# Optimization experiments

Measured on AMD Instinct MI355X. Metric: run time of the kernel, lower is better.

Reference implementation:

```python
import jax, jax.numpy as jnp
import numpy as np

N_NODES = 100000
N_EDGES = 3200000


def _gcn_conv(x, src, dst, W, b, n_nodes):
    # PyG GCNConv: out = D^{-1/2} (A + I) D^{-1/2} X W + b
    h = x @ W  # [N, out]
    # degree of (A + I) counted at targets (symmetric graph assumption as in PyG norm)
    deg = jax.ops.segment_sum(jnp.ones_like(dst, dtype=h.dtype), dst, num_segments=n_nodes)
    dinv = jnp.where(deg > 0, jax.lax.rsqrt(deg), 0.0)
    norm = dinv[src] * dinv[dst]  # [E_total]
    msg = h[src] * norm[:, None]  # gather + normalize  [E_total, out]
    out = jax.ops.segment_sum(msg, dst, num_segments=n_nodes)  # scatter-add
    return out + b


def setup_inputs() -> dict:
    key = jax.random.key(0)
    k1, k2, k3, k4 = jax.random.split(key, 4)
    x = jax.random.normal(k1, (N_NODES, 1), dtype=jnp.float32)
    edge_index = jax.random.randint(k2, (2, N_EDGES), 0, N_NODES, dtype=jnp.int64)
    W1 = jax.random.normal(k3, (1, 64), dtype=jnp.float32) * (1.0 / np.sqrt(1.0))
    b1 = jnp.zeros((64,), dtype=jnp.float32)
    W2 = jax.random.normal(k4, (64, 2), dtype=jnp.float32) * (1.0 / np.sqrt(64.0))
    b2 = jnp.zeros((2,), dtype=jnp.float32)
    return {"x": x, "edge_index": edge_index, "W1": W1, "b1": b1, "W2": W2, "b2": b2}


def reference(x, edge_index, W1, b1, W2, b2):
    n = x.shape[0]
    # add self-loops as GCNConv does by default
    loops = jnp.arange(n, dtype=edge_index.dtype)
    src = jnp.concatenate([edge_index[0], loops])
    dst = jnp.concatenate([edge_index[1], loops])
    h = _gcn_conv(x, src, dst, W1, b1, n)
    h = jax.nn.relu(h)
    h = _gcn_conv(h, src, dst, W2, b2, n)
    h = jax.nn.log_softmax(h, axis=1)
    out = jnp.mean(h, axis=0)
    return out[None, :]  # [1, 2]
```

## Files before the change

### kernel.cpp

```cpp
#include <hip/hip_runtime.h>


#define TPB 256
#define SORT_BLK 256
#define BSHIFT 7
#define BNODES 128
#define MAXBUCK 1024
#define BSTRIDE 6144


__global__ __launch_bounds__(TPB) void k_sort(const int* __restrict__ ei, int E, int epb,
                                              int nbuck, int* __restrict__ gcur,
                                              unsigned* __restrict__ packed) {
    __shared__ int h[MAXBUCK];
    for (int b = threadIdx.x; b < nbuck; b += TPB) h[b] = 0;
    __syncthreads();
    const int4* d4 = (const int4*)(ei + E);
    int nq = epb >> 2;
    int q0 = blockIdx.x * nq;
    for (int j = threadIdx.x; j < nq; j += TPB) {
        int q = q0 + j;
        int e = q << 2;
        if (e + 3 < E) {
            int4 v = d4[q];
            atomicAdd(&h[v.x >> BSHIFT], 1);
            atomicAdd(&h[v.y >> BSHIFT], 1);
            atomicAdd(&h[v.z >> BSHIFT], 1);
            atomicAdd(&h[v.w >> BSHIFT], 1);
        } else {
            for (int k = 0; k < 4; ++k)
                if (e + k < E) atomicAdd(&h[(ei + E)[e + k] >> BSHIFT], 1);
        }
    }
    __syncthreads();
    for (int b = threadIdx.x; b < nbuck; b += TPB) {
        int c = h[b];
        h[b] = c ? atomicAdd(&gcur[b], c) : 0;
    }
    __syncthreads();
    const int4* s4 = (const int4*)ei;
    for (int j = threadIdx.x; j < nq; j += TPB) {
        int q = q0 + j;
        int e = q << 2;
        if (e + 3 < E) {
            int4 vs = s4[q];
            int4 vd = d4[q];
            int b, p;
            b = vd.x >> BSHIFT; p = atomicAdd(&h[b], 1);
            packed[b * BSTRIDE + p] = ((unsigned)(vd.x & (BNODES - 1)) << 17) | (unsigned)vs.x;
            b = vd.y >> BSHIFT; p = atomicAdd(&h[b], 1);
            packed[b * BSTRIDE + p] = ((unsigned)(vd.y & (BNODES - 1)) << 17) | (unsigned)vs.y;
            b = vd.z >> BSHIFT; p = atomicAdd(&h[b], 1);
            packed[b * BSTRIDE + p] = ((unsigned)(vd.z & (BNODES - 1)) << 17) | (unsigned)vs.z;
            b = vd.w >> BSHIFT; p = atomicAdd(&h[b], 1);
            packed[b * BSTRIDE + p] = ((unsigned)(vd.w & (BNODES - 1)) << 17) | (unsigned)vs.w;
        } else {
            for (int k = 0; k < 4; ++k) {
                int ee = e + k;
                if (ee < E) {
                    int s = ei[ee], d = ei[E + ee];
                    int b = d >> BSHIFT;
                    int p = atomicAdd(&h[b], 1);
                    packed[b * BSTRIDE + p] = ((unsigned)(d & (BNODES - 1)) << 17) | (unsigned)s;
                }
            }
        }
    }
}


__global__ __launch_bounds__(TPB) void k_deg_u(const unsigned* __restrict__ packed,
                                               const int* __restrict__ gcur,
                                               const float* __restrict__ x,
                                               float* __restrict__ dinv,
                                               float* __restrict__ u, int N) {
    __shared__ int cnt[4][BNODES];
    for (int k = threadIdx.x; k < 4 * BNODES; k += TPB) ((int*)cnt)[k] = 0;
    __syncthreads();
    int b = blockIdx.x;
    int sz = gcur[b];
    const unsigned* base = packed + (size_t)b * BSTRIDE;
    const uint4* base4 = (const uint4*)base;
    int wv = threadIdx.x >> 6;
    int nq = sz >> 2;
    for (int j = threadIdx.x; j < nq; j += TPB) {
        uint4 p = base4[j];
        atomicAdd(&cnt[wv][(p.x >> 17) & 127], 1);
        atomicAdd(&cnt[wv][(p.y >> 17) & 127], 1);
        atomicAdd(&cnt[wv][(p.z >> 17) & 127], 1);
        atomicAdd(&cnt[wv][(p.w >> 17) & 127], 1);
    }
    int tail = sz & 3;
    if (threadIdx.x < tail) {
        unsigned p = base[(nq << 2) + threadIdx.x];
        atomicAdd(&cnt[wv][(p >> 17) & 127], 1);
    }
    __syncthreads();
    if (threadIdx.x < BNODES) {
        int t = threadIdx.x;
        int node = (b << BSHIFT) + t;
        if (node < N) {
            int deg = cnt[0][t] + cnt[1][t] + cnt[2][t] + cnt[3][t];
            float di = rsqrtf((float)(deg + 1));
            dinv[node] = di;
            u[node] = di * x[node];
        }
    }
}

__global__ __launch_bounds__(TPB) void k_agg1(const unsigned* __restrict__ packed,
                                              const int* __restrict__ gcur,
                                              const float* __restrict__ dinv,
                                              const float* __restrict__ u,
                                              const float* __restrict__ W1,
                                              const float* __restrict__ b1,
                                              const float* __restrict__ W2,
                                              float2* __restrict__ w, int N) {
    __shared__ float acc[4][BNODES];
    __shared__ float sW1[64], sb1[64], sW2[128];
    if (threadIdx.x < 64) { sW1[threadIdx.x] = W1[threadIdx.x]; sb1[threadIdx.x] = b1[threadIdx.x]; }
    if (threadIdx.x < 128) sW2[threadIdx.x] = W2[threadIdx.x];
    for (int k = threadIdx.x; k < 4 * BNODES; k += TPB) ((float*)acc)[k] = 0.f;
    __syncthreads();
    int b = blockIdx.x;
    int sz = gcur[b];
    const unsigned* base = packed + (size_t)b * BSTRIDE;
    const uint4* base4 = (const uint4*)base;
    int wv = threadIdx.x >> 6;
    int nq = sz >> 2;
    for (int j = threadIdx.x; j < nq; j += TPB) {
        uint4 p = base4[j];
        float v0 = u[p.x & 0x1FFFF];
        float v1 = u[p.y & 0x1FFFF];
        float v2 = u[p.z & 0x1FFFF];
        float v3 = u[p.w & 0x1FFFF];
        atomicAdd(&acc[wv][(p.x >> 17) & 127], v0);
        atomicAdd(&acc[wv][(p.y >> 17) & 127], v1);
        atomicAdd(&acc[wv][(p.z >> 17) & 127], v2);
        atomicAdd(&acc[wv][(p.w >> 17) & 127], v3);
    }
    int tail = sz & 3;
    if (threadIdx.x < tail) {
        unsigned p = base[(nq << 2) + threadIdx.x];
        atomicAdd(&acc[wv][(p >> 17) & 127], u[p & 0x1FFFF]);
    }
    __syncthreads();
    if (threadIdx.x < BNODES) {
        int t = threadIdx.x;
        int node = (b << BSHIFT) + t;
        if (node < N) {
            float di = dinv[node];
            float sv = di * (acc[0][t] + acc[1][t] + acc[2][t] + acc[3][t] + u[node]);
            float z0 = 0.f, z1 = 0.f;
            #pragma unroll
            for (int j = 0; j < 64; ++j) {
                float h = fmaxf(fmaf(sv, sW1[j], sb1[j]), 0.f);
                z0 = fmaf(h, sW2[2 * j], z0);
                z1 = fmaf(h, sW2[2 * j + 1], z1);
            }
            w[node] = make_float2(di * z0, di * z1);
        }
    }
}

__global__ __launch_bounds__(TPB) void k_agg2(const unsigned* __restrict__ packed,
                                              const int* __restrict__ gcur,
                                              const float* __restrict__ dinv,
                                              const float2* __restrict__ w,
                                              const float* __restrict__ b2,
                                              float* __restrict__ accum, int N) {
    __shared__ float accx[4][BNODES], accy[4][BNODES];
    for (int k = threadIdx.x; k < 4 * BNODES; k += TPB) {
        ((float*)accx)[k] = 0.f;
        ((float*)accy)[k] = 0.f;
    }
    __syncthreads();
    int b = blockIdx.x;
    int sz = gcur[b];
    const unsigned* base = packed + (size_t)b * BSTRIDE;
    const uint4* base4 = (const uint4*)base;
    int wv = threadIdx.x >> 6;
    int nq = sz >> 2;
    for (int j = threadIdx.x; j < nq; j += TPB) {
        uint4 p = base4[j];
        float2 v0 = w[p.x & 0x1FFFF];
        float2 v1 = w[p.y & 0x1FFFF];
        float2 v2 = w[p.z & 0x1FFFF];
        float2 v3 = w[p.w & 0x1FFFF];
        int l0 = (p.x >> 17) & 127, l1 = (p.y >> 17) & 127;
        int l2 = (p.z >> 17) & 127, l3 = (p.w >> 17) & 127;
        atomicAdd(&accx[wv][l0], v0.x); atomicAdd(&accy[wv][l0], v0.y);
        atomicAdd(&accx[wv][l1], v1.x); atomicAdd(&accy[wv][l1], v1.y);
        atomicAdd(&accx[wv][l2], v2.x); atomicAdd(&accy[wv][l2], v2.y);
        atomicAdd(&accx[wv][l3], v3.x); atomicAdd(&accy[wv][l3], v3.y);
    }
    int tail = sz & 3;
    if (threadIdx.x < tail) {
        unsigned p = base[(nq << 2) + threadIdx.x];
        float2 v = w[p & 0x1FFFF];
        int l = (p >> 17) & 127;
        atomicAdd(&accx[wv][l], v.x);
        atomicAdd(&accy[wv][l], v.y);
    }
    __syncthreads();
    float l0 = 0.f, l1 = 0.f;
    if (threadIdx.x < BNODES) {
        int t = threadIdx.x;
        int node = (b << BSHIFT) + t;
        if (node < N) {
            float di = dinv[node];
            float2 wi = w[node];
            float a0 = di * (accx[0][t] + accx[1][t] + accx[2][t] + accx[3][t] + wi.x) + b2[0];
            float a1 = di * (accy[0][t] + accy[1][t] + accy[2][t] + accy[3][t] + wi.y) + b2[1];
            float m = fmaxf(a0, a1);
            float lse = m + logf(expf(a0 - m) + expf(a1 - m));
            l0 = a0 - lse;
            l1 = a1 - lse;
        }
    }
    #pragma unroll
    for (int off = 32; off > 0; off >>= 1) {
        l0 += __shfl_down(l0, off, 64);
        l1 += __shfl_down(l1, off, 64);
    }
    __shared__ float s0[TPB / 64], s1[TPB / 64];
    int wid = threadIdx.x >> 6, lane = threadIdx.x & 63;
    if (lane == 0) { s0[wid] = l0; s1[wid] = l1; }
    __syncthreads();
    if (threadIdx.x == 0) {
        float t0 = 0.f, t1 = 0.f;
        #pragma unroll
        for (int k = 0; k < TPB / 64; ++k) { t0 += s0[k]; t1 += s1[k]; }
        atomicAdd(&accum[0], t0);
        atomicAdd(&accum[1], t1);
    }
}

__global__ void k_finalize(const float* __restrict__ accum, float* __restrict__ out, float invN) {
    out[0] = accum[0] * invN;
    out[1] = accum[1] * invN;
}


__global__ void k_hist(const int* __restrict__ dst, int E, int* __restrict__ deg) {
    int e = blockIdx.x * TPB + threadIdx.x;
    if (e < E) atomicAdd(&deg[dst[e]], 1);
}
__global__ void k_dinv_u(const int* __restrict__ deg, const float* __restrict__ x,
                         float* __restrict__ dinv, float* __restrict__ u, int N) {
    int i = blockIdx.x * TPB + threadIdx.x;
    if (i < N) {
        float di = rsqrtf((float)(deg[i] + 1));
        dinv[i] = di;
        u[i] = di * x[i];
    }
}
__global__ void k_scatter1(const int* __restrict__ ei, int E,
                           const float* __restrict__ u, float* __restrict__ t) {
    int e = blockIdx.x * TPB + threadIdx.x;
    if (e < E) atomicAdd(&t[ei[E + e]], u[ei[e]]);
}
__global__ void k_node_mid_fb(const float* __restrict__ dinv, const float* __restrict__ u,
                              const float* __restrict__ t,
                              const float* __restrict__ W1, const float* __restrict__ b1,
                              const float* __restrict__ W2, float2* __restrict__ w, int N) {
    __shared__ float sW1[64], sb1[64], sW2[128];
    if (threadIdx.x < 64) { sW1[threadIdx.x] = W1[threadIdx.x]; sb1[threadIdx.x] = b1[threadIdx.x]; }
    if (threadIdx.x < 128) sW2[threadIdx.x] = W2[threadIdx.x];
    __syncthreads();
    int i = blockIdx.x * TPB + threadIdx.x;
    if (i < N) {
        float di = dinv[i];
        float s = di * (t[i] + u[i]);
        float z0 = 0.f, z1 = 0.f;
        #pragma unroll
        for (int j = 0; j < 64; ++j) {
            float h = fmaxf(fmaf(s, sW1[j], sb1[j]), 0.f);
            z0 = fmaf(h, sW2[2 * j], z0);
            z1 = fmaf(h, sW2[2 * j + 1], z1);
        }
        w[i] = make_float2(di * z0, di * z1);
    }
}
__global__ void k_scatter2(const int* __restrict__ ei, int E,
                           const float2* __restrict__ w, float* __restrict__ acc) {
    int e = blockIdx.x * TPB + threadIdx.x;
    if (e < E) {
        float2 ws = w[ei[e]];
        int d = ei[E + e];
        atomicAdd(&acc[2 * d], ws.x);
        atomicAdd(&acc[2 * d + 1], ws.y);
    }
}
__global__ void k_node_out_fb(const float* __restrict__ dinv, const float2* __restrict__ w,
                              const float2* __restrict__ acc, const float* __restrict__ b2,
                              float* __restrict__ accum, int N) {
    int i = blockIdx.x * TPB + threadIdx.x;
    float l0 = 0.f, l1 = 0.f;
    if (i < N) {
        float di = dinv[i];
        float2 a = acc[i];
        float2 ww = w[i];
        float a0 = di * (a.x + ww.x) + b2[0];
        float a1 = di * (a.y + ww.y) + b2[1];
        float m = fmaxf(a0, a1);
        float lse = m + logf(expf(a0 - m) + expf(a1 - m));
        l0 = a0 - lse;
        l1 = a1 - lse;
    }
    #pragma unroll
    for (int off = 32; off > 0; off >>= 1) {
        l0 += __shfl_down(l0, off, 64);
        l1 += __shfl_down(l1, off, 64);
    }
    __shared__ float s0[TPB / 64], s1[TPB / 64];
    int wid = threadIdx.x >> 6, lane = threadIdx.x & 63;
    if (lane == 0) { s0[wid] = l0; s1[wid] = l1; }
    __syncthreads();
    if (threadIdx.x == 0) {
        float t0 = 0.f, t1 = 0.f;
        #pragma unroll
        for (int k = 0; k < TPB / 64; ++k) { t0 += s0[k]; t1 += s1[k]; }
        atomicAdd(&accum[0], t0);
        atomicAdd(&accum[1], t1);
    }
}

extern "C" void kernel_launch(void* const* d_in, const int* in_sizes, int n_in,
                              void* d_out, int out_size, void* d_ws, size_t ws_size,
                              hipStream_t stream) {
    const float* x  = (const float*)d_in[0];
    const int*   ei = (const int*)d_in[1];
    const float* W1 = (const float*)d_in[2];
    const float* b1 = (const float*)d_in[3];
    const float* W2 = (const float*)d_in[4];
    const float* b2 = (const float*)d_in[5];
    float* out = (float*)d_out;

    const int N = in_sizes[0];
    const int E = in_sizes[1] / 2;
    const int nbuck = (N + BNODES - 1) >> BSHIFT;
    const int gridN = (N + TPB - 1) / TPB;
    const int gridE = (E + TPB - 1) / TPB;

    size_t offPacked = 0;
    size_t offW      = offPacked + (size_t)nbuck * BSTRIDE * 4;
    size_t offDinv   = offW + (size_t)N * 8;
    size_t offU      = offDinv + (size_t)N * 4;
    size_t offGcur   = offU + (size_t)N * 4;
    size_t offAccum  = offGcur + (size_t)nbuck * 4;
    size_t need      = offAccum + 8;

    if (ws_size >= need && nbuck <= MAXBUCK && N <= (1 << 17)) {
        unsigned* packed = (unsigned*)((char*)d_ws + offPacked);
        float2*   w      = (float2*)((char*)d_ws + offW);
        float*    dinv   = (float*)((char*)d_ws + offDinv);
        float*    u      = (float*)((char*)d_ws + offU);
        int*      gcur   = (int*)((char*)d_ws + offGcur);
        float*    accum  = (float*)((char*)d_ws + offAccum);

        hipMemsetAsync(gcur, 0, (size_t)nbuck * 4 + 8, stream);

        int epb = (((E + SORT_BLK - 1) / SORT_BLK) + 3) & ~3;

        k_sort<<<SORT_BLK, TPB, 0, stream>>>(ei, E, epb, nbuck, gcur, packed);
        k_deg_u<<<nbuck, TPB, 0, stream>>>(packed, gcur, x, dinv, u, N);
        k_agg1<<<nbuck, TPB, 0, stream>>>(packed, gcur, dinv, u, W1, b1, W2, w, N);
        k_agg2<<<nbuck, TPB, 0, stream>>>(packed, gcur, dinv, (const float2*)w, b2, accum, N);
        k_finalize<<<1, 64, 0, stream>>>(accum, out, 1.0f / (float)N);
    } else {
        int*   deg   = (int*)d_ws;
        float* t     = (float*)(deg + N);
        float* acc   = t + N;
        float* accum = acc + 2 * N;
        float* dinv  = accum + 2;
        float* u     = dinv + N;
        float2* w    = (float2*)(u + N);
        hipMemsetAsync(d_ws, 0, (size_t)(4 * N + 2) * sizeof(float), stream);
        k_hist<<<gridE, TPB, 0, stream>>>(ei + E, E, deg);
        k_dinv_u<<<gridN, TPB, 0, stream>>>(deg, x, dinv, u, N);
        k_scatter1<<<gridE, TPB, 0, stream>>>(ei, E, u, t);
        k_node_mid_fb<<<gridN, TPB, 0, stream>>>(dinv, u, t, W1, b1, W2, w, N);
        k_scatter2<<<gridE, TPB, 0, stream>>>(ei, E, w, acc);
        k_node_out_fb<<<gridN, TPB, 0, stream>>>(dinv, w, (const float2*)acc, b2, accum, N);
        k_finalize<<<1, 64, 0, stream>>>(accum, out, 1.0f / (float)N);
    }
}
```

Before: 193.7 us.

## Sub-sort buckets by source chunk and stage gathers through shared memory

The degree kernel now also sorts each destination bucket's edges by source-node chunk of 4096 nodes and records per-bucket chunk offsets. Both aggregation kernels walk the chunks, stage the chunk's u or w values into LDS, and gather from LDS instead of doing random global loads. The aim is to replace scattered global gathers with coalesced staging loads. The cost is that every block stages all 25 chunks (about 100K floats or float2s per block across roughly 780 blocks), which adds a lot of redundant global traffic, plus extra syncs, a serial scan, and the loss of uint4-vectorised edge reads.

```diff
diff --git a/kernel.cpp b/kernel.cpp
--- a/kernel.cpp
+++ b/kernel.cpp
@@ -7,6 +7,9 @@
 #define BNODES 128
 #define MAXBUCK 1024
 #define BSTRIDE 6144
+#define CSHIFT 12
+#define CSZ 4096
+#define MAXCHUNK 32
 
 
 __global__ __launch_bounds__(TPB) void k_sort(const int* __restrict__ ei, int E, int epb,
@@ -69,53 +72,75 @@
 }
 
 
-__global__ __launch_bounds__(TPB) void k_deg_u(const unsigned* __restrict__ packed,
+__global__ __launch_bounds__(TPB) void k_sort2(unsigned* __restrict__ packed,
                                                const int* __restrict__ gcur,
                                                const float* __restrict__ x,
                                                float* __restrict__ dinv,
-                                               float* __restrict__ u, int N) {
-    __shared__ int cnt[4][BNODES];
-    for (int k = threadIdx.x; k < 4 * BNODES; k += TPB) ((int*)cnt)[k] = 0;
+                                               float* __restrict__ u,
+                                               int* __restrict__ chunkOff,
+                                               int nchunk, int N) {
+    __shared__ unsigned wbuf[BSTRIDE];
+    __shared__ int cntc[4][MAXCHUNK];
+    __shared__ int cntd[4][BNODES];
+    __shared__ int scanA[MAXCHUNK + 1];
+    __shared__ int cur[MAXCHUNK];
+    int wv = threadIdx.x >> 6;
+    for (int k = threadIdx.x; k < 4 * MAXCHUNK; k += TPB) ((int*)cntc)[k] = 0;
+    for (int k = threadIdx.x; k < 4 * BNODES; k += TPB) ((int*)cntd)[k] = 0;
     __syncthreads();
     int b = blockIdx.x;
     int sz = gcur[b];
-    const unsigned* base = packed + (size_t)b * BSTRIDE;
-    const uint4* base4 = (const uint4*)base;
-    int wv = threadIdx.x >> 6;
-    int nq = sz >> 2;
-    for (int j = threadIdx.x; j < nq; j += TPB) {
-        uint4 p = base4[j];
-        atomicAdd(&cnt[wv][(p.x >> 17) & 127], 1);
-        atomicAdd(&cnt[wv][(p.y >> 17) & 127], 1);
-        atomicAdd(&cnt[wv][(p.z >> 17) & 127], 1);
-        atomicAdd(&cnt[wv][(p.w >> 17) & 127], 1);
-    }
-    int tail = sz & 3;
-    if (threadIdx.x < tail) {
-        unsigned p = base[(nq << 2) + threadIdx.x];
-        atomicAdd(&cnt[wv][(p >> 17) & 127], 1);
+    unsigned* gbase = packed + (size_t)b * BSTRIDE;
+    for (int j = threadIdx.x; j < sz; j += TPB) {
+        unsigned wd = gbase[j];
+        wbuf[j] = wd;
+        atomicAdd(&cntc[wv][(wd & 0x1FFFF) >> CSHIFT], 1);
+        atomicAdd(&cntd[wv][(wd >> 17) & 127], 1);
     }
     __syncthreads();
     if (threadIdx.x < BNODES) {
         int t = threadIdx.x;
         int node = (b << BSHIFT) + t;
         if (node < N) {
-            int deg = cnt[0][t] + cnt[1][t] + cnt[2][t] + cnt[3][t];
+            int deg = cntd[0][t] + cntd[1][t] + cntd[2][t] + cntd[3][t];
             float di = rsqrtf((float)(deg + 1));
             dinv[node] = di;
             u[node] = di * x[node];
         }
     }
-}
+    if (threadIdx.x == 0) {
+        int run = 0;
+        for (int c = 0; c < nchunk; ++c) {
+            int v = cntc[0][c] + cntc[1][c] + cntc[2][c] + cntc[3][c];
+            scanA[c] = run;
+            run += v;
+        }
+        scanA[nchunk] = run;
+    }
+    __syncthreads();
+    if (threadIdx.x <= nchunk)
+        chunkOff[b * (MAXCHUNK + 1) + threadIdx.x] = scanA[threadIdx.x];
+    if (threadIdx.x < nchunk) cur[threadIdx.x] = scanA[threadIdx.x];
+    __syncthreads();
+    for (int j = threadIdx.x; j < sz; j += TPB) {
+        unsigned wd = wbuf[j];
+        int c = (wd & 0x1FFFF) >> CSHIFT;
+        int p = atomicAdd(&cur[c], 1);
+        gbase[p] = wd;
+    }
+}
+
 
 __global__ __launch_bounds__(TPB) void k_agg1(const unsigned* __restrict__ packed,
-                                              const int* __restrict__ gcur,
+                                              const int* __restrict__ chunkOff,
                                               const float* __restrict__ dinv,
                                               const float* __restrict__ u,
                                               const float* __restrict__ W1,
                                               const float* __restrict__ b1,
                                               const float* __restrict__ W2,
-                                              float2* __restrict__ w, int N) {
+                                              float2* __restrict__ w,
+                                              int nchunk, int N) {
+    __shared__ float uStage[CSZ];
     __shared__ float acc[4][BNODES];
     __shared__ float sW1[64], sb1[64], sW2[128];
     if (threadIdx.x < 64) { sW1[threadIdx.x] = W1[threadIdx.x]; sb1[threadIdx.x] = b1[threadIdx.x]; }
@@ -123,28 +148,26 @@
     for (int k = threadIdx.x; k < 4 * BNODES; k += TPB) ((float*)acc)[k] = 0.f;
     __syncthreads();
     int b = blockIdx.x;
-    int sz = gcur[b];
-    const unsigned* base = packed + (size_t)b * BSTRIDE;
-    const uint4* base4 = (const uint4*)base;
+    const unsigned* gbase = packed + (size_t)b * BSTRIDE;
+    const int* off = chunkOff + b * (MAXCHUNK + 1);
     int wv = threadIdx.x >> 6;
-    int nq = sz >> 2;
-    for (int j = threadIdx.x; j < nq; j += TPB) {
-        uint4 p = base4[j];
-        float v0 = u[p.x & 0x1FFFF];
-        float v1 = u[p.y & 0x1FFFF];
-        float v2 = u[p.z & 0x1FFFF];
-        float v3 = u[p.w & 0x1FFFF];
-        atomicAdd(&acc[wv][(p.x >> 17) & 127], v0);
-        atomicAdd(&acc[wv][(p.y >> 17) & 127], v1);
-        atomicAdd(&acc[wv][(p.z >> 17) & 127], v2);
-        atomicAdd(&acc[wv][(p.w >> 17) & 127], v3);
-    }
-    int tail = sz & 3;
-    if (threadIdx.x < tail) {
-        unsigned p = base[(nq << 2) + threadIdx.x];
-        atomicAdd(&acc[wv][(p >> 17) & 127], u[p & 0x1FFFF]);
-    }
-    __syncthreads();
+    for (int c = 0; c < nchunk; ++c) {
+        int o0 = off[c], o1 = off[c + 1];
+        if (o0 == o1) continue;
+        int gb = c << CSHIFT;
+        #pragma unroll
+        for (int k = 0; k < CSZ / TPB; ++k) {
+            int idx = gb + threadIdx.x + k * TPB;
+            uStage[threadIdx.x + k * TPB] = (idx < N) ? u[idx] : 0.f;
+        }
+        __syncthreads();
+        for (int j = o0 + threadIdx.x; j < o1; j += TPB) {
+            unsigned wd = gbase[j];
+            float v = uStage[wd & (CSZ - 1)];
+            atomicAdd(&acc[wv][(wd >> 17) & 127], v);
+        }
+        __syncthreads();
+    }
     if (threadIdx.x < BNODES) {
         int t = threadIdx.x;
         int node = (b << BSHIFT) + t;
@@ -163,12 +186,15 @@
     }
 }
 
+
 __global__ __launch_bounds__(TPB) void k_agg2(const unsigned* __restrict__ packed,
-                                              const int* __restrict__ gcur,
+                                              const int* __restrict__ chunkOff,
                                               const float* __restrict__ dinv,
                                               const float2* __restrict__ w,
                                               const float* __restrict__ b2,
-                                              float* __restrict__ accum, int N) {
+                                              float* __restrict__ accum,
+                                              int nchunk, int N) {
+    __shared__ float2 wStage[CSZ];
     __shared__ float accx[4][BNODES], accy[4][BNODES];
     for (int k = threadIdx.x; k < 4 * BNODES; k += TPB) {
         ((float*)accx)[k] = 0.f;
@@ -176,33 +202,28 @@
     }
     __syncthreads();
     int b = blockIdx.x;
-    int sz = gcur[b];
-    const unsigned* base = packed + (size_t)b * BSTRIDE;
-    const uint4* base4 = (const uint4*)base;
+    const unsigned* gbase = packed + (size_t)b * BSTRIDE;
+    const int* off = chunkOff + b * (MAXCHUNK + 1);
     int wv = threadIdx.x >> 6;
-    int nq = sz >> 2;
-    for (int j = threadIdx.x; j < nq; j += TPB) {
-        uint4 p = base4[j];
-        float2 v0 = w[p.x & 0x1FFFF];
-        float2 v1 = w[p.y & 0x1FFFF];
-        float2 v2 = w[p.z & 0x1FFFF];
-        float2 v3 = w[p.w & 0x1FFFF];
-        int l0 = (p.x >> 17) & 127, l1 = (p.y >> 17) & 127;
-        int l2 = (p.z >> 17) & 127, l3 = (p.w >> 17) & 127;
-        atomicAdd(&accx[wv][l0], v0.x); atomicAdd(&accy[wv][l0], v0.y);
-        atomicAdd(&accx[wv][l1], v1.x); atomicAdd(&accy[wv][l1], v1.y);
-        atomicAdd(&accx[wv][l2], v2.x); atomicAdd(&accy[wv][l2], v2.y);
-        atomicAdd(&accx[wv][l3], v3.x); atomicAdd(&accy[wv][l3], v3.y);
-    }
-    int tail = sz & 3;
-    if (threadIdx.x < tail) {
-        unsigned p = base[(nq << 2) + threadIdx.x];
-        float2 v = w[p & 0x1FFFF];
-        int l = (p >> 17) & 127;
-        atomicAdd(&accx[wv][l], v.x);
-        atomicAdd(&accy[wv][l], v.y);
-    }
-    __syncthreads();
+    for (int c = 0; c < nchunk; ++c) {
+        int o0 = off[c], o1 = off[c + 1];
+        if (o0 == o1) continue;
+        int gb = c << CSHIFT;
+        #pragma unroll
+        for (int k = 0; k < CSZ / TPB; ++k) {
+            int idx = gb + threadIdx.x + k * TPB;
+            wStage[threadIdx.x + k * TPB] = (idx < N) ? w[idx] : make_float2(0.f, 0.f);
+        }
+        __syncthreads();
+        for (int j = o0 + threadIdx.x; j < o1; j += TPB) {
+            unsigned wd = gbase[j];
+            float2 v = wStage[wd & (CSZ - 1)];
+            int l = (wd >> 17) & 127;
+            atomicAdd(&accx[wv][l], v.x);
+            atomicAdd(&accy[wv][l], v.y);
+        }
+        __syncthreads();
+    }
     float l0 = 0.f, l1 = 0.f;
     if (threadIdx.x < BNODES) {
         int t = threadIdx.x;
@@ -219,9 +240,9 @@
         }
     }
     #pragma unroll
-    for (int off = 32; off > 0; off >>= 1) {
-        l0 += __shfl_down(l0, off, 64);
-        l1 += __shfl_down(l1, off, 64);
+    for (int off2 = 32; off2 > 0; off2 >>= 1) {
+        l0 += __shfl_down(l0, off2, 64);
+        l1 += __shfl_down(l1, off2, 64);
     }
     __shared__ float s0[TPB / 64], s1[TPB / 64];
     int wid = threadIdx.x >> 6, lane = threadIdx.x & 63;
@@ -340,6 +361,7 @@
     const int N = in_sizes[0];
     const int E = in_sizes[1] / 2;
     const int nbuck = (N + BNODES - 1) >> BSHIFT;
+    const int nchunk = (N + CSZ - 1) >> CSHIFT;
     const int gridN = (N + TPB - 1) / TPB;
     const int gridE = (E + TPB - 1) / TPB;
 
@@ -349,24 +371,26 @@
     size_t offU      = offDinv + (size_t)N * 4;
     size_t offGcur   = offU + (size_t)N * 4;
     size_t offAccum  = offGcur + (size_t)nbuck * 4;
-    size_t need      = offAccum + 8;
-
-    if (ws_size >= need && nbuck <= MAXBUCK && N <= (1 << 17)) {
-        unsigned* packed = (unsigned*)((char*)d_ws + offPacked);
-        float2*   w      = (float2*)((char*)d_ws + offW);
-        float*    dinv   = (float*)((char*)d_ws + offDinv);
-        float*    u      = (float*)((char*)d_ws + offU);
-        int*      gcur   = (int*)((char*)d_ws + offGcur);
-        float*    accum  = (float*)((char*)d_ws + offAccum);
+    size_t offCOff   = offAccum + 8;
+    size_t need      = offCOff + (size_t)nbuck * (MAXCHUNK + 1) * 4;
+
+    if (ws_size >= need && nbuck <= MAXBUCK && N <= (1 << 17) && nchunk <= MAXCHUNK) {
+        unsigned* packed   = (unsigned*)((char*)d_ws + offPacked);
+        float2*   w        = (float2*)((char*)d_ws + offW);
+        float*    dinv     = (float*)((char*)d_ws + offDinv);
+        float*    u        = (float*)((char*)d_ws + offU);
+        int*      gcur     = (int*)((char*)d_ws + offGcur);
+        float*    accum    = (float*)((char*)d_ws + offAccum);
+        int*      chunkOff = (int*)((char*)d_ws + offCOff);
 
         hipMemsetAsync(gcur, 0, (size_t)nbuck * 4 + 8, stream);
 
         int epb = (((E + SORT_BLK - 1) / SORT_BLK) + 3) & ~3;
 
         k_sort<<<SORT_BLK, TPB, 0, stream>>>(ei, E, epb, nbuck, gcur, packed);
-        k_deg_u<<<nbuck, TPB, 0, stream>>>(packed, gcur, x, dinv, u, N);
-        k_agg1<<<nbuck, TPB, 0, stream>>>(packed, gcur, dinv, u, W1, b1, W2, w, N);
-        k_agg2<<<nbuck, TPB, 0, stream>>>(packed, gcur, dinv, (const float2*)w, b2, accum, N);
+        k_sort2<<<nbuck, TPB, 0, stream>>>(packed, gcur, x, dinv, u, chunkOff, nchunk, N);
+        k_agg1<<<nbuck, TPB, 0, stream>>>(packed, chunkOff, dinv, u, W1, b1, W2, w, nchunk, N);
+        k_agg2<<<nbuck, TPB, 0, stream>>>(packed, chunkOff, dinv, (const float2*)w, b2, accum, nchunk, N);
         k_finalize<<<1, 64, 0, stream>>>(accum, out, 1.0f / (float)N);
     } else {
         int*   deg   = (int*)d_ws;
```

Measured after the change: 376.7 us. +94.4%, slower.
